# Optimization experiments

Measured on AMD Instinct MI355X. Metric: run time of the kernel, lower is better.

## Reference

```python
import jax, jax.numpy as jnp
import numpy as np

MID = 256

def setup_inputs() -> dict:
    key = jax.random.key(0)
    ks = jax.random.split(key, 6)
    s = 1.0 / np.sqrt(MID)
    u = lambda k, shape: jax.random.uniform(k, shape, jnp.float32, -s, s)
    return {
        "W_ih": u(ks[0], (4 * MID, 2)),
        "W_hh": u(ks[1], (4 * MID, MID)),
        "b_ih": u(ks[2], (4 * MID,)),
        "b_hh": u(ks[3], (4 * MID,)),
        "W_out": u(ks[4], (1, MID)),
        "b_out": u(ks[5], (1,)),
        "sequence_dim": 48,
        "sequence_num": 512,
    }

def reference(W_ih, W_hh, b_ih, b_hh, W_out, b_out, sequence_dim, sequence_num):
    # obs is 2-D -> torch nn.LSTM treats it as UNBATCHED: (L=sequence_num, H_in=2),
    # hidden state (mid,) per layer, carried across outer iterations.
    N = sequence_num
    mid = W_hh.shape[1]
    b = b_ih + b_hh  # fuse the two LSTM biases

    def lstm(hc, obs):
        # obs: (N, 2) time-major unbatched sequence
        def step(carry, x):
            h, c = carry
            g = W_ih @ x + W_hh @ h + b          # (4*mid,)
            i, f, gg, o = jnp.split(g, 4)         # torch gate order i,f,g,o
            c = jax.nn.sigmoid(f) * c + jax.nn.sigmoid(i) * jnp.tanh(gg)
            h = jax.nn.sigmoid(o) * jnp.tanh(c)
            return (h, c), h
        hc, hs = jax.lax.scan(step, hc, obs)
        return hc, hs                              # hs: (N, mid)

    def outer(carry, k):
        hc, samp, prob = carry
        obs = jnp.concatenate([samp, prob], axis=1)  # (N, 2)
        hc, hs = lstm(hc, obs)
        p = jax.nn.sigmoid(hs @ W_out.T + b_out)     # (N, 1)
        smp = jax.random.bernoulli(k, p).astype(p.dtype)
        lp = smp * jnp.log(p) + (1.0 - smp) * jnp.log1p(-p)        # Bernoulli log_prob
        ent = -(p * jnp.log(p) + (1.0 - p) * jnp.log1p(-p))        # Bernoulli entropy
        return (hc, smp, p), (smp[:, 0], lp[:, 0], ent[:, 0])

    key = jax.random.key(42)
    keys = jax.random.split(key, sequence_dim - 1)
    h0 = (jnp.zeros((mid,), W_hh.dtype), jnp.zeros((mid,), W_hh.dtype))
    z = jnp.zeros((N, 1), W_hh.dtype)
    _, (ss, lps, ents) = jax.lax.scan(outer, (h0, z, z), keys)

    samples = jnp.concatenate([jnp.zeros((1, N), ss.dtype), ss], axis=0)  # (T, N)
    samples = samples.T.astype(jnp.int32)                                  # (N, T)
    logprobs = lps.sum(0)
    logprobs = logprobs - logprobs.mean()
    entropies = ents.mean(0)
    return samples, logprobs, entropies
```

## Files before the change

kernel.cpp:

```cpp
#include <hip/hip_runtime.h>
#include <stdint.h>


#define MID      256
#define NOUT     48
#define NSEQ     512
#define NOUTER   47
#define NSTEP    (NOUTER * NSEQ)
#define NBLK     16
#define HPER     16
#define MAGIC_V  0x1234ABCDu

__device__ __forceinline__ uint32_t rotl32(uint32_t x, int d) {
  return (x << d) | (x >> (32 - d));
}

__device__ __forceinline__ void threefry2x32(uint32_t k0, uint32_t k1,
                                             uint32_t x0, uint32_t x1,
                                             uint32_t& o0, uint32_t& o1) {
  uint32_t ks2 = k0 ^ k1 ^ 0x1BD11BDAu;
  uint32_t v0 = x0 + k0, v1 = x1 + k1;
#define TF_R(r) { v0 += v1; v1 = rotl32(v1, r); v1 ^= v0; }
  TF_R(13) TF_R(15) TF_R(26) TF_R(6)
  v0 += k1;  v1 += ks2 + 1u;
  TF_R(17) TF_R(29) TF_R(16) TF_R(24)
  v0 += ks2; v1 += k0 + 2u;
  TF_R(13) TF_R(15) TF_R(26) TF_R(6)
  v0 += k0;  v1 += k1 + 3u;
  TF_R(17) TF_R(29) TF_R(16) TF_R(24)
  v0 += k1;  v1 += ks2 + 4u;
  TF_R(13) TF_R(15) TF_R(26) TF_R(6)
  v0 += ks2; v1 += k0 + 5u;
#undef TF_R
  o0 = v0; o1 = v1;
}

__device__ __forceinline__ float sigf(float x) { return 1.0f / (1.0f + expf(-x)); }

__device__ __forceinline__ uint64_t packht(float h, uint32_t tag) {
  return ((uint64_t)tag << 32) | (uint64_t)__float_as_uint(h);
}

__global__ __launch_bounds__(256, 1)
void arlstm_kernel(const float* __restrict__ W_ih, const float* __restrict__ W_hh,
                   const float* __restrict__ b_ih, const float* __restrict__ b_hh,
                   const float* __restrict__ W_out, const float* __restrict__ b_out,
                   float* __restrict__ out, uint64_t* __restrict__ ws) {
  uint64_t* h_slot = ws;
  uint64_t* h_hist = ws + 4 * 256;
  float*    obsbuf = (float*)(ws + 4 * 256 + 512 * 256);
  uint32_t* p_prog = (uint32_t*)(obsbuf + 2 * 512 * 2);
  uint32_t* magic  = p_prog + 16;

  const int tid = threadIdx.x;
  const int blk = blockIdx.x;

  __shared__ __align__(16) float hstage[256];
  __shared__ float plds[4][64];
  __shared__ float obs_lds[2];
  __shared__ float lp_acc[512];
  __shared__ float ent_acc[512];
  __shared__ float red[256];

  if (blk == NBLK) {
    __hip_atomic_store(&h_slot[tid], 0ull, __ATOMIC_RELAXED, __HIP_MEMORY_SCOPE_AGENT);
    if (tid < 16)
      __hip_atomic_store(&p_prog[tid], 0u, __ATOMIC_RELAXED, __HIP_MEMORY_SCOPE_AGENT);
    out[(tid)       * NOUT] = 0.0f;
    out[(tid + 256) * NOUT] = 0.0f;
    lp_acc[tid] = 0.0f;  lp_acc[tid + 256] = 0.0f;
    ent_acc[tid] = 0.0f; ent_acc[tid + 256] = 0.0f;
    __threadfence();
    __syncthreads();
    if (tid == 0)
      __hip_atomic_store(magic, MAGIC_V, __ATOMIC_RELEASE, __HIP_MEMORY_SCOPE_AGENT);

    const int w    = tid >> 6;
    const int lane = tid & 63;
    const float wo0 = W_out[lane * 4 + 0], wo1 = W_out[lane * 4 + 1];
    const float wo2 = W_out[lane * 4 + 2], wo3 = W_out[lane * 4 + 3];
    const float bo = b_out[0];

    for (int s = w + 1; s <= NSTEP; s += 4) {
      const int k = (s - 1) >> 9;
      const int t = (s - 1) & 511;
      uint64_t* src = h_hist + (uint64_t)(s & 511) * 256 + lane * 4;
      uint64_t v0, v1, v2, v3;
      for (;;) {
        v0 = __hip_atomic_load(src + 0, __ATOMIC_RELAXED, __HIP_MEMORY_SCOPE_AGENT);
        v1 = __hip_atomic_load(src + 1, __ATOMIC_RELAXED, __HIP_MEMORY_SCOPE_AGENT);
        v2 = __hip_atomic_load(src + 2, __ATOMIC_RELAXED, __HIP_MEMORY_SCOPE_AGENT);
        v3 = __hip_atomic_load(src + 3, __ATOMIC_RELAXED, __HIP_MEMORY_SCOPE_AGENT);
        int ok = ((uint32_t)(v0 >> 32) == (uint32_t)s) &
                 ((uint32_t)(v1 >> 32) == (uint32_t)s) &
                 ((uint32_t)(v2 >> 32) == (uint32_t)s) &
                 ((uint32_t)(v3 >> 32) == (uint32_t)s);
        if (__all(ok)) break;
      }
      float zp = fmaf(__uint_as_float((uint32_t)v0), wo0,
                 fmaf(__uint_as_float((uint32_t)v1), wo1,
                 fmaf(__uint_as_float((uint32_t)v2), wo2,
                      __uint_as_float((uint32_t)v3) * wo3)));
      zp += __shfl_xor(zp, 1);
      zp += __shfl_xor(zp, 2);
      zp += __shfl_xor(zp, 4);
      zp += __shfl_xor(zp, 8);
      zp += __shfl_xor(zp, 16);
      zp += __shfl_xor(zp, 32);
      const float p = sigf(zp + bo);

      uint32_t ka, kb, c1, c2;
      threefry2x32(0u, 42u, 0u, (uint32_t)k, ka, kb);
      threefry2x32(ka, kb, 0u, (uint32_t)t, c1, c2);
      const uint32_t bits = c1 ^ c2;
      const float u = __uint_as_float((bits >> 9) | 0x3f800000u) - 1.0f;
      const float smp = (u < p) ? 1.0f : 0.0f;

      if (lane == 0) {
        uint32_t* ob = (uint32_t*)(obsbuf + ((k + 1) & 1) * (512 * 2) + t * 2);
        __hip_atomic_store(&ob[0], __float_as_uint(smp), __ATOMIC_RELAXED, __HIP_MEMORY_SCOPE_AGENT);
        __hip_atomic_store(&ob[1], __float_as_uint(p),   __ATOMIC_RELAXED, __HIP_MEMORY_SCOPE_AGENT);
        __hip_atomic_store(&p_prog[w], (uint32_t)s, __ATOMIC_RELEASE, __HIP_MEMORY_SCOPE_AGENT);
        out[t * NOUT + (k + 1)] = smp;
        const float lg = logf(p), lg1 = log1pf(-p);
        lp_acc[t]  += (smp > 0.5f) ? lg : lg1;
        ent_acc[t] -= (p * lg + (1.0f - p) * lg1);
      }
    }
    __syncthreads();
    red[tid] = lp_acc[tid] + lp_acc[tid + 256];
    __syncthreads();
    for (int off = 128; off > 0; off >>= 1) {
      if (tid < off) red[tid] += red[tid + off];
      __syncthreads();
    }
    const float mean = red[0] * (1.0f / 512.0f);
    out[24576 + tid]        = lp_acc[tid]        - mean;
    out[24576 + 256 + tid]  = lp_acc[tid + 256]  - mean;
    out[25088 + tid]        = ent_acc[tid]       * (1.0f / 47.0f);
    out[25088 + 256 + tid]  = ent_acc[tid + 256] * (1.0f / 47.0f);
  } else {
    const int part = tid >> 6;
    const int r    = tid & 63;
    const int gate = r >> 4;
    const int jloc = r & 15;
    const int row  = gate * 256 + blk * HPER + jloc;

    float wreg[64];
#pragma unroll
    for (int c = 0; c < 64; ++c)
      wreg[c] = W_hh[row * 256 + part * 64 + c];

    float bi[4], wx0[4], wx1[4];
    if (tid < 16) {
#pragma unroll
      for (int g4 = 0; g4 < 4; ++g4) {
        const int rr = g4 * 256 + blk * HPER + tid;
        bi[g4]  = b_ih[rr] + b_hh[rr];
        wx0[g4] = W_ih[rr * 2 + 0];
        wx1[g4] = W_ih[rr * 2 + 1];
      }
    }

    if (tid == 0) {
      while (__hip_atomic_load(magic, __ATOMIC_ACQUIRE, __HIP_MEMORY_SCOPE_AGENT) != MAGIC_V) {}
    }
    __syncthreads();

    float c_st = 0.0f;
    const int jglob = blk * HPER + (tid & 15);

    for (int s = 1; s <= NSTEP; ++s) {
      const int k = (s - 1) >> 9;
      const int t = (s - 1) & 511;

      float samp = 0.0f, pv = 0.0f;
      if (tid == 255 && k > 0) {
        const uint32_t X = (uint32_t)((k - 1) * 512 + t + 1);
        while (__hip_atomic_load(&p_prog[t & 3], __ATOMIC_ACQUIRE, __HIP_MEMORY_SCOPE_AGENT) < X) {}
        uint32_t* ob = (uint32_t*)(obsbuf + (k & 1) * (512 * 2) + t * 2);
        samp = __uint_as_float(__hip_atomic_load(&ob[0], __ATOMIC_RELAXED, __HIP_MEMORY_SCOPE_AGENT));
        pv   = __uint_as_float(__hip_atomic_load(&ob[1], __ATOMIC_RELAXED, __HIP_MEMORY_SCOPE_AGENT));
      }

      {
        uint64_t* src = h_slot + (uint64_t)((s - 1) & 3) * 256 + tid;
        uint64_t v;
        do {
          v = __hip_atomic_load(src, __ATOMIC_RELAXED, __HIP_MEMORY_SCOPE_AGENT);
        } while ((uint32_t)(v >> 32) != (uint32_t)(s - 1));
        hstage[tid] = __uint_as_float((uint32_t)v);
      }
      if (tid == 255) { obs_lds[0] = samp; obs_lds[1] = pv; }
      __syncthreads();

      float a0 = 0.f, a1 = 0.f, a2 = 0.f, a3 = 0.f;
      const float4* hs4 = (const float4*)(hstage + part * 64);
#pragma unroll
      for (int i = 0; i < 16; ++i) {
        const float4 hv = hs4[i];
        a0 = fmaf(wreg[4 * i + 0], hv.x, a0);
        a1 = fmaf(wreg[4 * i + 1], hv.y, a1);
        a2 = fmaf(wreg[4 * i + 2], hv.z, a2);
        a3 = fmaf(wreg[4 * i + 3], hv.w, a3);
      }
      plds[part][r] = (a0 + a1) + (a2 + a3);
      __syncthreads();

      if (tid < 16) {
        const float sx = obs_lds[0], px = obs_lds[1];
        float g[4];
#pragma unroll
        for (int g4 = 0; g4 < 4; ++g4) {
          const int rr = g4 * 16 + tid;
          const float base = wx0[g4] * sx + wx1[g4] * px + bi[g4];
          g[g4] = ((plds[0][rr] + plds[1][rr]) + (plds[2][rr] + plds[3][rr])) + base;
        }
        const float ig = sigf(g[0]);
        const float fg = sigf(g[1]);
        const float gg = tanhf(g[2]);
        const float og = sigf(g[3]);
        const float t1 = fg * c_st;
        const float t2 = ig * gg;
        c_st = t1 + t2;
        const float hnew = og * tanhf(c_st);
        const uint64_t pk = packht(hnew, (uint32_t)s);
        __hip_atomic_store(&h_slot[(uint64_t)(s & 3) * 256 + jglob], pk,
                           __ATOMIC_RELAXED, __HIP_MEMORY_SCOPE_AGENT);
        __hip_atomic_store(&h_hist[(uint64_t)(s & 511) * 256 + jglob], pk,
                           __ATOMIC_RELAXED, __HIP_MEMORY_SCOPE_AGENT);
      }
    }
  }
}

extern "C" void kernel_launch(void* const* d_in, const int* in_sizes, int n_in,
                              void* d_out, int out_size, void* d_ws, size_t ws_size,
                              hipStream_t stream) {
  const float* W_ih  = (const float*)d_in[0];
  const float* W_hh  = (const float*)d_in[1];
  const float* b_ih  = (const float*)d_in[2];
  const float* b_hh  = (const float*)d_in[3];
  const float* W_out = (const float*)d_in[4];
  const float* b_out = (const float*)d_in[5];
  float* out = (float*)d_out;
  uint64_t* ws = (uint64_t*)d_ws;

  arlstm_kernel<<<dim3(NBLK + 1), dim3(256), 0, stream>>>(
      W_ih, W_hh, b_ih, b_hh, W_out, b_out, out, ws);
}
```

Baseline: 38.50 ms.

## Poll history buffer directly and parallelize gate activations across 64 lanes

Removes the separate 4-slot h ring and has consumers poll the 512-entry history buffer directly, so each step issues one store instead of two. Gate nonlinearities are now computed by 64 lanes using hardware exp2/rcp intrinsics, with shuffles gathering the results, instead of 16 lanes evaluating four expf/tanhf each. The spin-wait keeps two loads in flight. Fast approximate intrinsics may change numerics slightly, which could flip Bernoulli samples.

```diff
diff --git a/kernel.cpp b/kernel.cpp
--- a/kernel.cpp
+++ b/kernel.cpp
@@ -8,8 +8,8 @@
 #define NOUTER   47
 #define NSTEP    (NOUTER * NSEQ)
 #define NBLK     16
-#define HPER     16
 #define MAGIC_V  0x1234ABCDu
+#define LOG2E    1.4426950408889634f
 
 __device__ __forceinline__ uint32_t rotl32(uint32_t x, int d) {
   return (x << d) | (x >> (32 - d));
@@ -46,9 +46,8 @@
                    const float* __restrict__ b_ih, const float* __restrict__ b_hh,
                    const float* __restrict__ W_out, const float* __restrict__ b_out,
                    float* __restrict__ out, uint64_t* __restrict__ ws) {
-  uint64_t* h_slot = ws;
-  uint64_t* h_hist = ws + 4 * 256;
-  float*    obsbuf = (float*)(ws + 4 * 256 + 512 * 256);
+  uint64_t* h_hist = ws;
+  float*    obsbuf = (float*)(ws + 512 * 256);
   uint32_t* p_prog = (uint32_t*)(obsbuf + 2 * 512 * 2);
   uint32_t* magic  = p_prog + 16;
 
@@ -63,7 +62,7 @@
   __shared__ float red[256];
 
   if (blk == NBLK) {
-    __hip_atomic_store(&h_slot[tid], 0ull, __ATOMIC_RELAXED, __HIP_MEMORY_SCOPE_AGENT);
+    __hip_atomic_store(&h_hist[tid], 0ull, __ATOMIC_RELAXED, __HIP_MEMORY_SCOPE_AGENT);
     if (tid < 16)
       __hip_atomic_store(&p_prog[tid], 0u, __ATOMIC_RELAXED, __HIP_MEMORY_SCOPE_AGENT);
     out[(tid)       * NOUT] = 0.0f;
@@ -144,22 +143,23 @@
     const int r    = tid & 63;
     const int gate = r >> 4;
     const int jloc = r & 15;
-    const int row  = gate * 256 + blk * HPER + jloc;
+    const int row  = gate * 256 + blk * 16 + jloc;
 
     float wreg[64];
 #pragma unroll
     for (int c = 0; c < 64; ++c)
       wreg[c] = W_hh[row * 256 + part * 64 + c];
 
-    float bi[4], wx0[4], wx1[4];
-    if (tid < 16) {
-#pragma unroll
-      for (int g4 = 0; g4 < 4; ++g4) {
-        const int rr = g4 * 256 + blk * HPER + tid;
-        bi[g4]  = b_ih[rr] + b_hh[rr];
-        wx0[g4] = W_ih[rr * 2 + 0];
-        wx1[g4] = W_ih[rr * 2 + 1];
-      }
+    float bb = 0.f, wx0 = 0.f, wx1 = 0.f, mconst = 0.f, ml = 0.f, ad = 0.f;
+    if (tid < 64) {
+      const int g4 = tid >> 4;
+      const int rr = g4 * 256 + blk * 16 + (tid & 15);
+      bb  = b_ih[rr] + b_hh[rr];
+      wx0 = W_ih[rr * 2 + 0];
+      wx1 = W_ih[rr * 2 + 1];
+      mconst = (g4 == 2) ? (-2.0f * LOG2E) : (-LOG2E);
+      ml     = (g4 == 2) ? 2.0f : 1.0f;
+      ad     = (g4 == 2) ? -1.0f : 0.0f;
     }
 
     if (tid == 0) {
@@ -168,7 +168,7 @@
     __syncthreads();
 
     float c_st = 0.0f;
-    const int jglob = blk * HPER + (tid & 15);
+    const int jglob = blk * 16 + (tid & 15);
 
     for (int s = 1; s <= NSTEP; ++s) {
       const int k = (s - 1) >> 9;
@@ -184,11 +184,19 @@
       }
 
       {
-        uint64_t* src = h_slot + (uint64_t)((s - 1) & 3) * 256 + tid;
-        uint64_t v;
-        do {
-          v = __hip_atomic_load(src, __ATOMIC_RELAXED, __HIP_MEMORY_SCOPE_AGENT);
-        } while ((uint32_t)(v >> 32) != (uint32_t)(s - 1));
+        uint64_t* src = h_hist + (uint64_t)((s - 1) & 511) * 256 + tid;
+        const uint32_t want = (uint32_t)(s - 1);
+        uint64_t v = __hip_atomic_load(src, __ATOMIC_RELAXED, __HIP_MEMORY_SCOPE_AGENT);
+        if ((uint32_t)(v >> 32) != want) {
+          uint64_t a = __hip_atomic_load(src, __ATOMIC_RELAXED, __HIP_MEMORY_SCOPE_AGENT);
+          uint64_t b = __hip_atomic_load(src, __ATOMIC_RELAXED, __HIP_MEMORY_SCOPE_AGENT);
+          for (;;) {
+            if ((uint32_t)(a >> 32) == want) { v = a; break; }
+            a = __hip_atomic_load(src, __ATOMIC_RELAXED, __HIP_MEMORY_SCOPE_AGENT);
+            if ((uint32_t)(b >> 32) == want) { v = b; break; }
+            b = __hip_atomic_load(src, __ATOMIC_RELAXED, __HIP_MEMORY_SCOPE_AGENT);
+          }
+        }
         hstage[tid] = __uint_as_float((uint32_t)v);
       }
       if (tid == 255) { obs_lds[0] = samp; obs_lds[1] = pv; }
@@ -207,28 +215,30 @@
       plds[part][r] = (a0 + a1) + (a2 + a3);
       __syncthreads();
 
-      if (tid < 16) {
+      if (tid < 64) {
         const float sx = obs_lds[0], px = obs_lds[1];
-        float g[4];
-#pragma unroll
-        for (int g4 = 0; g4 < 4; ++g4) {
-          const int rr = g4 * 16 + tid;
-          const float base = wx0[g4] * sx + wx1[g4] * px + bi[g4];
-          g[g4] = ((plds[0][rr] + plds[1][rr]) + (plds[2][rr] + plds[3][rr])) + base;
+        const float base = wx0 * sx + wx1 * px + bb;
+        const float gv = ((plds[0][tid] + plds[1][tid]) +
+                          (plds[2][tid] + plds[3][tid])) + base;
+        const float e   = __builtin_amdgcn_exp2f(gv * mconst);
+        const float y   = __builtin_amdgcn_rcpf(1.0f + e);
+        const float act = __builtin_fmaf(ml, y, ad);
+        const int j = tid & 15;
+        const float a_f = __shfl(act, j + 16, 64);
+        const float a_g = __shfl(act, j + 32, 64);
+        const float a_o = __shfl(act, j + 48, 64);
+        if (tid < 16) {
+          const float t1 = a_f * c_st;
+          const float t2 = act * a_g;
+          c_st = t1 + t2;
+          const float ec = __builtin_amdgcn_exp2f(c_st * (-2.0f * LOG2E));
+          const float yc = __builtin_amdgcn_rcpf(1.0f + ec);
+          const float th = __builtin_fmaf(2.0f, yc, -1.0f);
+          const float hnew = a_o * th;
+          __hip_atomic_store(&h_hist[(uint64_t)(s & 511) * 256 + jglob],
+                             packht(hnew, (uint32_t)s),
+                             __ATOMIC_RELAXED, __HIP_MEMORY_SCOPE_AGENT);
         }
-        const float ig = sigf(g[0]);
-        const float fg = sigf(g[1]);
-        const float gg = tanhf(g[2]);
-        const float og = sigf(g[3]);
-        const float t1 = fg * c_st;
-        const float t2 = ig * gg;
-        c_st = t1 + t2;
-        const float hnew = og * tanhf(c_st);
-        const uint64_t pk = packht(hnew, (uint32_t)s);
-        __hip_atomic_store(&h_slot[(uint64_t)(s & 3) * 256 + jglob], pk,
-                           __ATOMIC_RELAXED, __HIP_MEMORY_SCOPE_AGENT);
-        __hip_atomic_store(&h_hist[(uint64_t)(s & 511) * 256 + jglob], pk,
-                           __ATOMIC_RELAXED, __HIP_MEMORY_SCOPE_AGENT);
       }
     }
   }
```

Result: faster. 31.76 ms (-17.5%).
